# Performance work log

Hardware: AMD Instinct MI355X
Metric: run time of the kernel (lower is better)

## Reference

```python
import jax, jax.numpy as jnp
import numpy as np

DIM = 32
B, H, W = 4, 256, 256


def conv1x1(x, w, b):
    # x: [B,C,H,W], w: [O,C], b: [O]
    return jnp.einsum('bchw,oc->bohw', x, w) + b[None, :, None, None]


def conv3x3(x, w, b):
    # x: [B,C,H,W], w: [O,C,3,3]
    out = jax.lax.conv_general_dilated(
        x, w, window_strides=(1, 1), padding='SAME',
        dimension_numbers=('NCHW', 'OIHW', 'NCHW'))
    return out + b[None, :, None, None]


def fft2d(x):
    # fft2 over last two dims, then fftshift over ALL dims (torch default)
    f = jnp.fft.fftshift(jnp.fft.fft2(x, norm='ortho'))
    return jnp.concatenate([f.real, f.imag], axis=1)  # [B,2C,H,W]


def ifft2d(x):
    f = jnp.fft.ifftshift(x)  # over ALL dims (torch default)
    re, im = jnp.split(f, 2, axis=1)
    c = jax.lax.complex(re, im)
    return jnp.abs(jnp.fft.ifft2(c, norm='ortho'))  # [B,C,H,W]


def setup_inputs() -> dict:
    key = jax.random.key(0)
    ks = jax.random.split(key, 16)
    C = DIM
    s = 0.02  # small init keeps the global-HW dot products in a sane softmax range
    inp = {
        'x': jax.random.normal(ks[0], (B, C, H, W), jnp.float32),
        'y': jax.random.normal(ks[1], (B, C, H, W), jnp.float32),
        'wq': jax.random.normal(ks[2], (C, C), jnp.float32) * s,
        'bq': jnp.zeros((C,), jnp.float32),
        'wk': jax.random.normal(ks[3], (C, C), jnp.float32) * s,
        'bk': jnp.zeros((C,), jnp.float32),
        'wv': jax.random.normal(ks[4], (C, C), jnp.float32) * s,
        'bv': jnp.zeros((C,), jnp.float32),
        'wd': jax.random.normal(ks[5], (C, C), jnp.float32) * s,
        'bd': jnp.zeros((C,), jnp.float32),
        'wc': jax.random.normal(ks[6], (2 * C, 2 * C, 3, 3), jnp.float32) * s,
        'bc': jnp.zeros((2 * C,), jnp.float32),
        'wi': jax.random.normal(ks[7], (2 * C, 2 * C, 3, 3), jnp.float32) * s,
        'bi': jnp.zeros((2 * C,), jnp.float32),
    }
    return inp


def reference(x, y, wq, bq, wk, bk, wv, bv, wd, bd, wc, bc, wi, bi):
    b, c, h, w = x.shape
    xq = conv1x1(x, wq, bq).reshape(b, c, h * w)            # [B,C,HW]
    dft = conv3x3(fft2d(conv1x1(y, wd, bd)), wc, bc)        # [B,2C,H,W]
    yk, yv = jnp.split(dft, 2, axis=1)
    yk = conv1x1(yk, wk, bk).reshape(b, c, h * w)
    yv = conv1x1(yv, wv, bv).reshape(b, c, h * w)
    att = jnp.einsum('bcn,bdn->bcd', xq, yk)                # [B,C,C]
    att = jax.nn.softmax(att, axis=1)                       # softmax over dim=1 (as in torch)
    out = jnp.einsum('bcd,bdn->bcn', att, yv).reshape(b, c, h, w)
    out = out + ifft2d(conv3x3(jax.nn.relu(dft), wi, bi))
    return out
```

## Files before the change

kernel.cpp:

```cpp
#include <hip/hip_runtime.h>
#include <math.h>

#define HW_ (256*256)
#define CH 32
#define CH2 64
#define BATCH 4

typedef short bf16x8 __attribute__((ext_vector_type(8)));
typedef float f32x4 __attribute__((ext_vector_type(4)));

__device__ __forceinline__ unsigned short f2bf(float f) {
    union { float f; unsigned u; } v; v.f = f;
    unsigned r = v.u + 0x7fffu + ((v.u >> 16) & 1u);
    return (unsigned short)(r >> 16);
}
__device__ __forceinline__ float bf2f(unsigned h) {
    union { unsigned u; float f; } v; v.u = h << 16;
    return v.f;
}

__device__ __forceinline__ int ctof_slot(int s) {
    return s < 16 ? s + 16 : s < 32 ? s + 32 : s < 48 ? s - 32 : s - 16;
}

__device__ __forceinline__ void build_tw4(float2* tw, float sign) {
    int tid = threadIdx.x;
    float ang = sign * 6.2831853071795864769f * (float)tid / 256.0f;
    float s, c; sincosf(ang, &s, &c);
    tw[tid] = make_float2(c, s);
}

__device__ __forceinline__ int rev4_8(int i) {
    return ((i & 3) << 6) | ((i & 12) << 2) | ((i & 48) >> 2) | (i >> 6);
}

__device__ __forceinline__ float2 cmul(float2 a, float2 b) {
    return make_float2(a.x*b.x - a.y*b.y, a.x*b.y + a.y*b.x);
}

template<int SGN>
__device__ __forceinline__ void fft_core4(float2* A, const float2* tw) {
    const int tid = threadIdx.x;
    for (int idx = tid; idx < 16*256; idx += 256) {
        int l = idx & 15, i = idx >> 4;
        int j = rev4_8(i);
        if (i < j) {
            int base = l*257;
            float2 t = A[base+i]; A[base+i] = A[base+j]; A[base+j] = t;
        }
    }
    __syncthreads();
    #pragma unroll
    for (int st = 0; st < 4; ++st) {
        const int lq2 = 2*st;
        const int q = 1 << lq2;
        const int estep = 64 >> lq2;
        for (int idx = tid; idx < 16*64; idx += 256) {
            int l = idx & 15, bf = idx >> 4;
            int j = bf & (q-1);
            int g = bf >> lq2;
            int base = l*257 + (g << (lq2+2)) + j;
            float2 x0 = A[base];
            float2 x1 = A[base + q];
            float2 x2 = A[base + 2*q];
            float2 x3 = A[base + 3*q];
            if (st > 0) {
                int e = j * estep;
                x1 = cmul(x1, tw[e]);
                x2 = cmul(x2, tw[2*e]);
                x3 = cmul(x3, tw[3*e]);
            }
            float2 t0 = make_float2(x0.x + x2.x, x0.y + x2.y);
            float2 t1 = make_float2(x0.x - x2.x, x0.y - x2.y);
            float2 t2 = make_float2(x1.x + x3.x, x1.y + x3.y);
            float2 t3 = make_float2(x1.x - x3.x, x1.y - x3.y);
            float2 r  = make_float2(-SGN * t3.y, SGN * t3.x);
            A[base]       = make_float2(t0.x + t2.x, t0.y + t2.y);
            A[base + q]   = make_float2(t1.x + r.x, t1.y + r.y);
            A[base + 2*q] = make_float2(t0.x - t2.x, t0.y - t2.y);
            A[base + 3*q] = make_float2(t1.x - r.x, t1.y - r.y);
        }
        __syncthreads();
    }
}

__global__ __launch_bounds__(256) void k_fft_fwd1(const unsigned short* __restrict__ yd, ushort2* __restrict__ CAt) {
    __shared__ float2 A[16*257];
    __shared__ float2 tw[256];
    build_tw4(tw, -1.0f);
    int blk = blockIdx.x;
    int bc = blk >> 4, h0 = (blk & 15) << 4;
    const float sc = 1.0f/16.0f;
    const unsigned short* src = yd + (size_t)bc*HW_ + (size_t)h0*256;
    for (int idx = threadIdx.x; idx < 16*256; idx += 256) {
        int l = idx >> 8, w = idx & 255;
        A[l*257 + w] = make_float2(bf2f(src[l*256 + w])*sc, 0.0f);
    }
    __syncthreads();
    fft_core4<-1>(A, tw);
    int t = threadIdx.x;
    ushort2* dst = CAt + (size_t)bc*HW_ + (size_t)t*256 + h0;
    #pragma unroll
    for (int l = 0; l < 16; ++l) {
        float2 v = A[l*257 + t];
        dst[l] = make_ushort2(f2bf(v.x), f2bf(v.y));
    }
}

__global__ __launch_bounds__(256) void k_fft_fwd2(const ushort2* __restrict__ CAt, unsigned short* __restrict__ FSH) {
    __shared__ float2 A[16*257];
    __shared__ float2 tw[256];
    build_tw4(tw, -1.0f);
    int blk = blockIdx.x;
    int b = blk >> 9, chalf = (blk >> 8) & 1, w = blk & 255;
    const float sc = 1.0f/16.0f;
    const ushort2* src = CAt + (((size_t)(b*32 + chalf*16))*256 + w)*256;
    for (int idx = threadIdx.x; idx < 16*256; idx += 256) {
        int l = idx >> 8, h = idx & 255;
        ushort2 v = src[(size_t)l*HW_ + h];
        A[l*257 + h] = make_float2(bf2f(v.x)*sc, bf2f(v.y)*sc);
    }
    __syncthreads();
    fft_core4<-1>(A, tw);
    int t = threadIdx.x;
    int bt = (b + 2) & 3;
    int ht = (t + 128) & 255;
    int wt = (w + 128) & 255;
    unsigned short pk[32];
    #pragma unroll
    for (int l = 0; l < 16; ++l) {
        float2 v = A[l*257 + t];
        pk[l]      = f2bf(v.x);
        pk[16 + l] = f2bf(v.y);
    }
    unsigned short* dst = FSH + ((((size_t)bt*256 + ht)*256 + wt)*64 + chalf*32);
    uint4* d4 = (uint4*)dst;
    const uint4* s4 = (const uint4*)pk;
    d4[0] = s4[0]; d4[1] = s4[1]; d4[2] = s4[2]; d4[3] = s4[3];
}

__global__ __launch_bounds__(256) void k_wpack2(const float* __restrict__ wc, const float* __restrict__ wi,
                                                unsigned short* __restrict__ d1, unsigned short* __restrict__ d2) {
    int i = blockIdx.x*256 + threadIdx.x;
    int half = i >= 36864;
    int j = i - half*36864;
    int tap = j >> 12, rem = j & 4095, oc = rem >> 6, s = rem & 63;
    if (half) {
        d2[j] = f2bf(wi[((size_t)(oc*64 + s))*9 + tap]);
    } else {
        int ic = ctof_slot(s);
        d1[j] = f2bf(wc[((size_t)(oc*64 + ic))*9 + tap]);
    }
}

template<int MODE>
__global__ __launch_bounds__(256) void k_conv3(const unsigned short* __restrict__ in_cl,
                                               const unsigned short* __restrict__ wpk,
                                               const float* __restrict__ bias,
                                               unsigned short* __restrict__ outp) {
    __shared__ __align__(16) char Xs[2112*16];
    __shared__ __align__(16) char Ws[1536*16];
    int tid = threadIdx.x;
    int blk = blockIdx.x;
    int wseg = blk & 3, hg = (blk >> 2) & 63, b = blk >> 8;
    int h0 = hg*4, w0 = wseg*64;

    const uint4* wsrc = (const uint4*)wpk;

    for (int gl = tid; gl < 2112; gl += 256) {
        int slot = gl / 528;
        int rem  = gl - slot*528;
        int col  = rem >> 3, hseg = rem & 7;
        int hh = h0 - 1 + slot;
        int wcol = w0 - 1 + col;
        uint4 v = make_uint4(0,0,0,0);
        if (hh >= 0 && hh < 256 && wcol >= 0 && wcol < 256) {
            v = *(const uint4*)(in_cl + (((size_t)(b*256 + hh)*256 + wcol)*64) + hseg*8);
            if (MODE == 1) {
                unsigned* pv = (unsigned*)&v;
                #pragma unroll
                for (int q = 0; q < 4; ++q) {
                    unsigned a = pv[q];
                    unsigned lo = a & 0xffffu, hi = a >> 16;
                    if (lo & 0x8000u) lo = 0;
                    if (hi & 0x8000u) hi = 0;
                    pv[q] = lo | (hi << 16);
                }
            }
        }
        *(uint4*)(Xs + ((gl << 4) ^ ((col & 7) << 4))) = v;
    }
    for (int gw = tid; gw < 1536; gw += 256) {
        int oc = (gw >> 3) & 63;
        *(uint4*)(Ws + ((gw << 4) ^ ((oc & 7) << 4))) = wsrc[gw];
    }
    __syncthreads();

    int lane = tid & 63;
    int wv = tid >> 6;
    int l16 = lane & 15, lq = lane >> 4;

    f32x4 acc[4][4];
    #pragma unroll
    for (int i = 0; i < 4; ++i)
        #pragma unroll
        for (int j = 0; j < 4; ++j) acc[i][j] = (f32x4)0.0f;

    for (int dy = 0; dy < 3; ++dy) {
        if (dy > 0) {
            __syncthreads();
            int k = dy + 3;
            int slot = k & 3;
            int hh = h0 - 1 + k;
            bool hv = hh < 256;
            for (int gl = tid; gl < 528; gl += 256) {
                int col = gl >> 3, hseg = gl & 7;
                int wcol = w0 - 1 + col;
                uint4 v = make_uint4(0,0,0,0);
                if (hv && wcol >= 0 && wcol < 256) {
                    v = *(const uint4*)(in_cl + (((size_t)(b*256 + hh)*256 + wcol)*64) + hseg*8);
                    if (MODE == 1) {
                        unsigned* pv = (unsigned*)&v;
                        #pragma unroll
                        for (int q = 0; q < 4; ++q) {
                            unsigned a = pv[q];
                            unsigned lo = a & 0xffffu, hi = a >> 16;
                            if (lo & 0x8000u) lo = 0;
                            if (hi & 0x8000u) hi = 0;
                            pv[q] = lo | (hi << 16);
                        }
                    }
                }
                int g = slot*528 + gl;
                *(uint4*)(Xs + ((g << 4) ^ ((col & 7) << 4))) = v;
            }
            for (int gw = tid; gw < 1536; gw += 256) {
                int oc = (gw >> 3) & 63;
                *(uint4*)(Ws + ((gw << 4) ^ ((oc & 7) << 4))) = wsrc[dy*1536 + gw];
            }
            __syncthreads();
        }
        int slot = (wv + dy) & 3;
        #pragma unroll
        for (int dx = 0; dx < 3; ++dx) {
            #pragma unroll
            for (int kk = 0; kk < 2; ++kk) {
                int hseg = kk*4 + lq;
                bf16x8 xf[4], wf[4];
                #pragma unroll
                for (int j = 0; j < 4; ++j) {
                    int col = j*16 + l16 + dx;
                    int g = slot*528 + col*8 + hseg;
                    xf[j] = *(const bf16x8*)(Xs + ((g << 4) ^ ((col & 7) << 4)));
                }
                #pragma unroll
                for (int i = 0; i < 4; ++i) {
                    int oc = i*16 + l16;
                    int lw = dx*512 + oc*8 + hseg;
                    wf[i] = *(const bf16x8*)(Ws + ((lw << 4) ^ ((oc & 7) << 4)));
                    #pragma unroll
                    for (int j = 0; j < 4; ++j) {
                        if (MODE == 0)
                            acc[i][j] = __builtin_amdgcn_mfma_f32_16x16x32_bf16(wf[i], xf[j], acc[i][j], 0, 0, 0);
                        else
                            acc[i][j] = __builtin_amdgcn_mfma_f32_16x16x32_bf16(xf[j], wf[i], acc[i][j], 0, 0, 0);
                    }
                }
            }
        }
    }

    int h = h0 + wv;
    if (MODE == 0) {
        #pragma unroll
        for (int j = 0; j < 4; ++j) {
            int px = w0 + j*16 + l16;
            unsigned short* orow = outp + (((size_t)b*256 + h)*256 + px)*64;
            #pragma unroll
            for (int i = 0; i < 4; ++i) {
                int oc0 = i*16 + lq*4;
                float4 bv = *(const float4*)(bias + oc0);
                unsigned short c0 = f2bf(acc[i][j][0] + bv.x);
                unsigned short c1 = f2bf(acc[i][j][1] + bv.y);
                unsigned short c2 = f2bf(acc[i][j][2] + bv.z);
                unsigned short c3 = f2bf(acc[i][j][3] + bv.w);
                uint2 u;
                u.x = (unsigned)c0 | ((unsigned)c1 << 16);
                u.y = (unsigned)c2 | ((unsigned)c3 << 16);
                *(uint2*)(orow + oc0) = u;
            }
        }
    } else {
        #pragma unroll
        for (int i = 0; i < 4; ++i) {
            int oc = i*16 + l16;
            float bv = bias[oc];
            unsigned short* oplane = outp + ((size_t)b*64 + oc)*HW_ + (size_t)h*256;
            #pragma unroll
            for (int j = 0; j < 4; ++j) {
                int px0 = w0 + j*16 + lq*4;
                unsigned short c0 = f2bf(acc[i][j][0] + bv);
                unsigned short c1 = f2bf(acc[i][j][1] + bv);
                unsigned short c2 = f2bf(acc[i][j][2] + bv);
                unsigned short c3 = f2bf(acc[i][j][3] + bv);
                uint2 u;
                u.x = (unsigned)c0 | ((unsigned)c1 << 16);
                u.y = (unsigned)c2 | ((unsigned)c3 << 16);
                *(uint2*)(oplane + px0) = u;
            }
        }
    }
}

__global__ __launch_bounds__(256) void k_conv1x1(const float* __restrict__ in, const float* __restrict__ w,
                                                 const float* __restrict__ bias, unsigned short* __restrict__ out) {
    __shared__ float ts[32*257];
    int blk = blockIdx.x; int b = blk >> 8, h = blk & 255;
    int tid = threadIdx.x;
    const float* src = in + (size_t)b*CH*HW_ + (size_t)h*256;
    for (int idx = tid; idx < 32*256; idx += 256) {
        int c = idx >> 8, ww = idx & 255;
        ts[c*257 + ww] = src[(size_t)c*HW_ + ww];
    }
    __syncthreads();
    float acc[32];
    #pragma unroll
    for (int o = 0; o < 32; ++o) acc[o] = bias[o];
    for (int c = 0; c < 32; ++c) {
        float v = ts[c*257 + tid];
        #pragma unroll
        for (int o = 0; o < 32; ++o) acc[o] += w[o*32 + c] * v;
    }
    unsigned short* dst = out + (size_t)b*CH*HW_ + (size_t)h*256 + tid;
    #pragma unroll
    for (int o = 0; o < 32; ++o) dst[(size_t)o*HW_] = f2bf(acc[o]);
}

__global__ __launch_bounds__(256) void k_gram(const float* __restrict__ x, const unsigned short* __restrict__ dcl,
                                              float* __restrict__ Mpart, float* __restrict__ Sxp, float* __restrict__ Sdp) {
    __shared__ float mred[1024];
    __shared__ float sxred[32];
    __shared__ float sdred[32];
    int blk = blockIdx.x;
    int b = blk >> 7, chunk = blk & 127;
    int tid = threadIdx.x, lane = tid & 63, wv = tid >> 6;
    int l16 = lane & 15, lq = lane >> 4;
    for (int idx = tid; idx < 1024; idx += 256) mred[idx] = 0.0f;
    if (tid < 32) { sxred[tid] = 0.0f; sdred[tid] = 0.0f; }
    __syncthreads();

    const float* xb0 = x + (size_t)b*CH*HW_ + (size_t)l16*HW_;
    const float* xb1 = xb0 + (size_t)16*HW_;
    const unsigned short* db = dcl + (size_t)b*HW_*64;

    f32x4 acc[2][2];
    #pragma unroll
    for (int i = 0; i < 2; ++i)
        #pragma unroll
        for (int j = 0; j < 2; ++j) acc[i][j] = (f32x4)0.0f;
    float sx0 = 0, sx1 = 0, sd0 = 0, sd1 = 0;

    int pxw = chunk*512 + wv*128;
    #pragma unroll
    for (int ks = 0; ks < 4; ++ks) {
        int px = pxw + ks*32 + lq*8;
        float4 xa = *(const float4*)(xb0 + px);
        float4 xc = *(const float4*)(xb0 + px + 4);
        float4 ya = *(const float4*)(xb1 + px);
        float4 yc = *(const float4*)(xb1 + px + 4);
        bf16x8 a0, a1, b0, b1;
        const float* pxa = (const float*)&xa;
        const float* pxc = (const float*)&xc;
        const float* pya = (const float*)&ya;
        const float* pyc = (const float*)&yc;
        #pragma unroll
        for (int j = 0; j < 4; ++j) {
            a0[j]   = (short)f2bf(pxa[j]);  sx0 += pxa[j];
            a0[4+j] = (short)f2bf(pxc[j]);  sx0 += pxc[j];
            a1[j]   = (short)f2bf(pya[j]);  sx1 += pya[j];
            a1[4+j] = (short)f2bf(pyc[j]);  sx1 += pyc[j];
        }
        const unsigned short* dbp = db + (size_t)px*64 + l16;
        #pragma unroll
        for (int j = 0; j < 8; ++j) {
            unsigned short v0 = dbp[j*64];
            unsigned short v1 = dbp[j*64 + 16];
            b0[j] = (short)v0;  sd0 += bf2f(v0);
            b1[j] = (short)v1;  sd1 += bf2f(v1);
        }
        acc[0][0] = __builtin_amdgcn_mfma_f32_16x16x32_bf16(a0, b0, acc[0][0], 0, 0, 0);
        acc[0][1] = __builtin_amdgcn_mfma_f32_16x16x32_bf16(a0, b1, acc[0][1], 0, 0, 0);
        acc[1][0] = __builtin_amdgcn_mfma_f32_16x16x32_bf16(a1, b0, acc[1][0], 0, 0, 0);
        acc[1][1] = __builtin_amdgcn_mfma_f32_16x16x32_bf16(a1, b1, acc[1][1], 0, 0, 0);
    }

    #pragma unroll
    for (int fi = 0; fi < 2; ++fi)
        #pragma unroll
        for (int fj = 0; fj < 2; ++fj)
            #pragma unroll
            for (int r = 0; r < 4; ++r)
                atomicAdd(&mred[(fi*16 + lq*4 + r)*32 + fj*16 + l16], acc[fi][fj][r]);

    sx0 += __shfl_xor(sx0, 16); sx0 += __shfl_xor(sx0, 32);
    sx1 += __shfl_xor(sx1, 16); sx1 += __shfl_xor(sx1, 32);
    sd0 += __shfl_xor(sd0, 16); sd0 += __shfl_xor(sd0, 32);
    sd1 += __shfl_xor(sd1, 16); sd1 += __shfl_xor(sd1, 32);
    if (lane < 16) {
        atomicAdd(&sxred[l16], sx0);
        atomicAdd(&sxred[l16 + 16], sx1);
        atomicAdd(&sdred[l16], sd0);
        atomicAdd(&sdred[l16 + 16], sd1);
    }
    __syncthreads();

    float* mp = Mpart + ((size_t)(b*128 + chunk))*1024;
    for (int idx = tid; idx < 1024; idx += 256) mp[idx] = mred[idx];
    if (tid < 32) {
        Sxp[(b*128 + chunk)*32 + tid] = sxred[tid];
        Sdp[(b*128 + chunk)*32 + tid] = sdred[tid];
    }
}

__global__ __launch_bounds__(256) void k_reduce(const float* __restrict__ Mpart, const float* __restrict__ Sxp,
                                                const float* __restrict__ Sdp,
                                                float* __restrict__ M, float* __restrict__ Sx, float* __restrict__ Sdk) {
    int b = blockIdx.x >> 2, seg = blockIdx.x & 3;
    int o = seg*256 + threadIdx.x;
    float s = 0;
    for (int c = 0; c < 128; ++c) s += Mpart[((size_t)(b*128 + c))*1024 + o];
    M[b*1024 + o] = s;
    if (seg == 0) {
        if (threadIdx.x < 32) {
            float t = 0;
            for (int c = 0; c < 128; ++c) t += Sxp[(b*128 + c)*32 + threadIdx.x];
            Sx[b*32 + threadIdx.x] = t;
        } else if (threadIdx.x < 64) {
            int e = threadIdx.x - 32;
            float t = 0;
            for (int c = 0; c < 128; ++c) t += Sdp[(b*128 + c)*32 + e];
            Sdk[b*32 + e] = t;
        }
    }
}

__global__ __launch_bounds__(256) void k_att(const float* __restrict__ M, const float* __restrict__ Sx,
                                              const float* __restrict__ Sdk,
                                              const float* __restrict__ wq, const float* __restrict__ bq,
                                              const float* __restrict__ wk, const float* __restrict__ bk,
                                              const float* __restrict__ wv, const float* __restrict__ bv,
                                              float* __restrict__ att2, float* __restrict__ sout) {
    __shared__ float Mls[1024], T1[1024], attls[32*33];
    __shared__ float wqs[1024], wks[1024], wvs[1024];
    __shared__ float q1[32], k1[32];
    int tid = threadIdx.x;
    int b = blockIdx.x;
    for (int idx = tid; idx < 1024; idx += 256) {
        wqs[idx] = wq[idx]; wks[idx] = wk[idx]; wvs[idx] = wv[idx];
        Mls[idx] = M[b*1024 + idx];
    }
    __syncthreads();
    if (tid < 32) { float s=0; for (int a=0;a<32;++a) s += wqs[tid*32+a]*Sx[b*32+a]; q1[tid]=s; }
    else if (tid < 64) { int d=tid-32; float s=0; for (int e=0;e<32;++e) s += wks[d*32+e]*Sdk[b*32+e]; k1[d]=s; }
    for (int idx = tid; idx < 1024; idx += 256) {
        int c = idx >> 5, e = idx & 31;
        float s = 0;
        for (int a=0;a<32;++a) s += wqs[c*32+a]*Mls[a*32+e];
        T1[idx] = s;
    }
    __syncthreads();
    for (int idx = tid; idx < 1024; idx += 256) {
        int c = idx >> 5, d = idx & 31;
        float s = 0;
        for (int e=0;e<32;++e) s += T1[c*32+e]*wks[d*32+e];
        s += bq[c]*k1[d] + bk[d]*q1[c] + 65536.0f*bq[c]*bk[d];
        attls[c*33+d] = s;
    }
    __syncthreads();
    if (tid < 32) {
        int d = tid;
        float mx = -1e30f;
        for (int c=0;c<32;++c) mx = fmaxf(mx, attls[c*33+d]);
        float sum = 0;
        for (int c=0;c<32;++c) { float e_ = expf(attls[c*33+d]-mx); attls[c*33+d]=e_; sum+=e_; }
        float inv = 1.0f/sum;
        for (int c=0;c<32;++c) attls[c*33+d] *= inv;
    }
    __syncthreads();
    for (int idx = tid; idx < 1024; idx += 256) {
        int c = idx >> 5, e = idx & 31;
        float s = 0;
        for (int d=0; d<32; ++d) s += attls[c*33+d]*wvs[d*32+e];
        att2[b*1024 + idx] = s;
    }
    if (tid < 32) {
        float s=0; for (int d=0;d<32;++d) s += attls[tid*33+d]*bv[d];
        sout[b*32+tid] = s;
    }
}

__global__ __launch_bounds__(256) void k_fft_inv1(const unsigned short* __restrict__ G, ushort2* __restrict__ Z1T) {
    __shared__ float2 A[16*257];
    __shared__ float2 tw[256];
    build_tw4(tw, 1.0f);
    int blk = blockIdx.x;
    int bc = blk >> 4, w0 = (blk & 15) << 4;
    int b = bc >> 5, c = bc & 31;
    int bs = (b + 2) & 3;
    const float sc = 1.0f/16.0f;
    const unsigned short* gre = G + ((size_t)(bs*CH2 + c + 32))*HW_;
    const unsigned short* gim = G + ((size_t)(bs*CH2 + c))*HW_;
    for (int idx = threadIdx.x; idx < 16*256; idx += 256) {
        int h = idx >> 4, l = idx & 15;
        int hs = (h + 128) & 255;
        int ws = (w0 + l + 128) & 255;
        A[l*257 + h] = make_float2(bf2f(gre[(size_t)hs*256 + ws])*sc, bf2f(gim[(size_t)hs*256 + ws])*sc);
    }
    __syncthreads();
    fft_core4<1>(A, tw);
    ushort2* dst = Z1T + (size_t)bc*HW_;
    for (int idx = threadIdx.x; idx < 16*256; idx += 256) {
        int l = idx >> 8, h = idx & 255;
        float2 v = A[l*257 + h];
        dst[(size_t)(w0 + l)*256 + h] = make_ushort2(f2bf(v.x), f2bf(v.y));
    }
}

__global__ __launch_bounds__(256) void k_fft_inv2(const ushort2* __restrict__ Z1T, float* __restrict__ out) {
    __shared__ float2 A[16*257];
    __shared__ float2 tw[256];
    build_tw4(tw, 1.0f);
    int blk = blockIdx.x;
    int bc = blk >> 4, h0 = (blk & 15) << 4;
    const float sc = 1.0f/16.0f;
    const ushort2* src = Z1T + (size_t)bc*HW_ + h0;
    for (int idx = threadIdx.x; idx < 16*256; idx += 256) {
        int w = idx >> 4, l = idx & 15;
        ushort2 v = src[(size_t)w*256 + l];
        A[l*257 + w] = make_float2(bf2f(v.x)*sc, bf2f(v.y)*sc);
    }
    __syncthreads();
    fft_core4<1>(A, tw);
    float* dst = out + (size_t)bc*HW_ + (size_t)h0*256;
    for (int idx = threadIdx.x; idx < 16*256; idx += 256) {
        int l = idx >> 8, w = idx & 255;
        float2 v = A[l*257 + w];
        dst[l*256 + w] = sqrtf(v.x*v.x + v.y*v.y);
    }
}

__global__ __launch_bounds__(256) void k_out(const unsigned short* __restrict__ dcl, const float* __restrict__ att2,
                                             const float* __restrict__ sv, float* __restrict__ out) {
    __shared__ __align__(16) float A2ls[1024];
    __shared__ float svls[32];
    int blk = blockIdx.x; int b = blk >> 8, h = blk & 255;
    int tid = threadIdx.x;
    for (int idx = tid; idx < 1024; idx += 256) A2ls[idx] = att2[b*1024 + idx];
    if (tid < 32) svls[tid] = sv[b*32 + tid];
    __syncthreads();
    int px = tid;
    const uint4* dvp = (const uint4*)(dcl + ((((size_t)b*256 + h)*256 + px)*64 + 32));
    uint4 d0 = dvp[0], d1 = dvp[1];
    unsigned u[8] = {d0.x, d0.y, d0.z, d0.w, d1.x, d1.y, d1.z, d1.w};
    float dv[32];
    #pragma unroll
    for (int i = 0; i < 8; ++i) {
        dv[2*i]   = bf2f(u[i] & 0xffffu);
        dv[2*i+1] = bf2f(u[i] >> 16);
    }
    float accv[32];
    #pragma unroll
    for (int c = 0; c < 32; ++c) accv[c] = svls[c];
    #pragma unroll
    for (int q = 0; q < 8; ++q) {
        #pragma unroll
        for (int c = 0; c < 32; ++c) {
            float4 a4 = *(const float4*)&A2ls[c*32 + q*4];
            accv[c] += a4.x*dv[q*4] + a4.y*dv[q*4+1] + a4.z*dv[q*4+2] + a4.w*dv[q*4+3];
        }
    }
    float* ob = out + (size_t)b*CH*HW_ + (size_t)h*256 + px;
    #pragma unroll
    for (int c = 0; c < 32; ++c) ob[(size_t)c*HW_] += accv[c];
}

extern "C" void kernel_launch(void* const* d_in, const int* in_sizes, int n_in,
                              void* d_out, int out_size, void* d_ws, size_t ws_size,
                              hipStream_t stream) {
    const float* x  = (const float*)d_in[0];
    const float* y  = (const float*)d_in[1];
    const float* wq = (const float*)d_in[2];
    const float* bq = (const float*)d_in[3];
    const float* wk = (const float*)d_in[4];
    const float* bk = (const float*)d_in[5];
    const float* wv = (const float*)d_in[6];
    const float* bv = (const float*)d_in[7];
    const float* wd = (const float*)d_in[8];
    const float* bd = (const float*)d_in[9];
    const float* wc = (const float*)d_in[10];
    const float* bc = (const float*)d_in[11];
    const float* wi = (const float*)d_in[12];
    const float* bi = (const float*)d_in[13];
    float* out = (float*)d_out;

    char* ws = (char*)d_ws;
    size_t o = 0;
    unsigned short* R1   = (unsigned short*)(ws + o); o += (size_t)BATCH*CH*HW_*2;
    ushort2*        CAt  = (ushort2*)(ws + o);        o += (size_t)BATCH*CH*HW_*4;
    unsigned short* FSHc = (unsigned short*)(ws + o); o += (size_t)BATCH*CH2*HW_*2;
    unsigned short* DFTc = (unsigned short*)(ws + o); o += (size_t)BATCH*CH2*HW_*2;
    unsigned short* Gpl  = (unsigned short*)(ws + o); o += (size_t)BATCH*CH2*HW_*2;
    unsigned short* wpk1 = (unsigned short*)(ws + o); o += 9*64*64*2;
    unsigned short* wpk2 = (unsigned short*)(ws + o); o += 9*64*64*2;
    float*          Mpart= (float*)(ws + o);          o += (size_t)512*1024*4;
    float*          Sxp  = (float*)(ws + o);          o += 512*32*4;
    float*          Sdp  = (float*)(ws + o);          o += 512*32*4;
    float*          Mb   = (float*)(ws + o);          o += 4096*4;
    float*          Sxb  = (float*)(ws + o);          o += 128*4;
    float*          Sdb  = (float*)(ws + o);          o += 128*4;
    float*          A2b  = (float*)(ws + o);          o += 4096*4;
    float*          Svb  = (float*)(ws + o);          o += 128*4;
    if (ws_size < o) return;

    ushort2* Z1T = CAt;

    k_wpack2<<<288, 256, 0, stream>>>(wc, wi, wpk1, wpk2);
    k_conv1x1<<<1024, 256, 0, stream>>>(y, wd, bd, R1);
    k_fft_fwd1<<<2048, 256, 0, stream>>>(R1, CAt);
    k_fft_fwd2<<<2048, 256, 0, stream>>>(CAt, FSHc);
    k_conv3<0><<<1024, 256, 0, stream>>>(FSHc, wpk1, bc, DFTc);
    k_conv3<1><<<1024, 256, 0, stream>>>(DFTc, wpk2, bi, Gpl);
    k_gram<<<512, 256, 0, stream>>>(x, DFTc, Mpart, Sxp, Sdp);
    k_reduce<<<16, 256, 0, stream>>>(Mpart, Sxp, Sdp, Mb, Sxb, Sdb);
    k_att<<<4, 256, 0, stream>>>(Mb, Sxb, Sdb, wq, bq, wk, bk, wv, bv, A2b, Svb);
    k_fft_inv1<<<2048, 256, 0, stream>>>(Gpl, Z1T);
    k_fft_inv2<<<2048, 256, 0, stream>>>(Z1T, out);
    k_out<<<1024, 256, 0, stream>>>(DFTc, A2b, Svb, out);
}
```

Baseline: 284.6 us.

## Register-based 16x16 FFT, direct-weight conv3, fuse reduce into att, bf16 magnitude buffer

Replaces the four-stage shared-memory radix-4 FFT, which had a bit-reversal pass and many barriers, with a two-pass 16x16 decomposition done in registers. Each pass uses one shared-memory transpose with diagonal skew. The 3x3 conv now loads all six input rows into shared memory once and reads weights straight from global memory, dropping the per-dy refill barriers and the weight staging buffer. The k_reduce kernel is folded into k_att. The inverse FFT magnitude is stored as bf16 and added in k_out instead of a read-modify-write of fp32 out. This trades more shared memory and global weight reads, plus extra rounding of the magnitude to bf16, for fewer syncs and fewer launches.

```diff
diff --git a/kernel.cpp b/kernel.cpp
--- a/kernel.cpp
+++ b/kernel.cpp
@@ -21,6 +21,10 @@
 
 __device__ __forceinline__ int ctof_slot(int s) {
     return s < 16 ? s + 16 : s < 32 ? s + 32 : s < 48 ? s - 32 : s - 16;
+}
+
+__device__ __forceinline__ float2 cmul(float2 a, float2 b) {
+    return make_float2(a.x*b.x - a.y*b.y, a.x*b.y + a.y*b.x);
 }
 
 __device__ __forceinline__ void build_tw4(float2* tw, float sign) {
@@ -30,58 +34,63 @@
     tw[tid] = make_float2(c, s);
 }
 
-__device__ __forceinline__ int rev4_8(int i) {
-    return ((i & 3) << 6) | ((i & 12) << 2) | ((i & 48) >> 2) | (i >> 6);
-}
-
-__device__ __forceinline__ float2 cmul(float2 a, float2 b) {
-    return make_float2(a.x*b.x - a.y*b.y, a.x*b.y + a.y*b.x);
-}
-
 template<int SGN>
-__device__ __forceinline__ void fft_core4(float2* A, const float2* tw) {
+__device__ __forceinline__ void fft16_reg(float2* x, const float2* tw) {
+    float2 u[16];
+    #pragma unroll
+    for (int m0 = 0; m0 < 4; ++m0) {
+        float2 x0 = x[m0], x1 = x[m0+4], x2 = x[m0+8], x3 = x[m0+12];
+        float2 t0 = make_float2(x0.x+x2.x, x0.y+x2.y);
+        float2 t1 = make_float2(x0.x-x2.x, x0.y-x2.y);
+        float2 t2 = make_float2(x1.x+x3.x, x1.y+x3.y);
+        float2 t3 = make_float2(x1.x-x3.x, x1.y-x3.y);
+        float2 r  = make_float2(-SGN*t3.y, SGN*t3.x);
+        u[m0*4+0] = make_float2(t0.x+t2.x, t0.y+t2.y);
+        u[m0*4+1] = make_float2(t1.x+r.x,  t1.y+r.y);
+        u[m0*4+2] = make_float2(t0.x-t2.x, t0.y-t2.y);
+        u[m0*4+3] = make_float2(t1.x-r.x,  t1.y-r.y);
+    }
+    #pragma unroll
+    for (int m0 = 1; m0 < 4; ++m0)
+        #pragma unroll
+        for (int a = 1; a < 4; ++a)
+            u[m0*4+a] = cmul(u[m0*4+a], tw[(16*m0*a) & 255]);
+    #pragma unroll
+    for (int a = 0; a < 4; ++a) {
+        float2 x0 = u[a], x1 = u[4+a], x2 = u[8+a], x3 = u[12+a];
+        float2 t0 = make_float2(x0.x+x2.x, x0.y+x2.y);
+        float2 t1 = make_float2(x0.x-x2.x, x0.y-x2.y);
+        float2 t2 = make_float2(x1.x+x3.x, x1.y+x3.y);
+        float2 t3 = make_float2(x1.x-x3.x, x1.y-x3.y);
+        float2 r  = make_float2(-SGN*t3.y, SGN*t3.x);
+        x[a]    = make_float2(t0.x+t2.x, t0.y+t2.y);
+        x[a+4]  = make_float2(t1.x+r.x,  t1.y+r.y);
+        x[a+8]  = make_float2(t0.x-t2.x, t0.y-t2.y);
+        x[a+12] = make_float2(t1.x-r.x,  t1.y-r.y);
+    }
+}
+
+template<int SGN>
+__device__ __forceinline__ void fft_core16(float2* A, const float2* tw) {
     const int tid = threadIdx.x;
-    for (int idx = tid; idx < 16*256; idx += 256) {
-        int l = idx & 15, i = idx >> 4;
-        int j = rev4_8(i);
-        if (i < j) {
-            int base = l*257;
-            float2 t = A[base+i]; A[base+i] = A[base+j]; A[base+j] = t;
-        }
-    }
-    __syncthreads();
-    #pragma unroll
-    for (int st = 0; st < 4; ++st) {
-        const int lq2 = 2*st;
-        const int q = 1 << lq2;
-        const int estep = 64 >> lq2;
-        for (int idx = tid; idx < 16*64; idx += 256) {
-            int l = idx & 15, bf = idx >> 4;
-            int j = bf & (q-1);
-            int g = bf >> lq2;
-            int base = l*257 + (g << (lq2+2)) + j;
-            float2 x0 = A[base];
-            float2 x1 = A[base + q];
-            float2 x2 = A[base + 2*q];
-            float2 x3 = A[base + 3*q];
-            if (st > 0) {
-                int e = j * estep;
-                x1 = cmul(x1, tw[e]);
-                x2 = cmul(x2, tw[2*e]);
-                x3 = cmul(x3, tw[3*e]);
-            }
-            float2 t0 = make_float2(x0.x + x2.x, x0.y + x2.y);
-            float2 t1 = make_float2(x0.x - x2.x, x0.y - x2.y);
-            float2 t2 = make_float2(x1.x + x3.x, x1.y + x3.y);
-            float2 t3 = make_float2(x1.x - x3.x, x1.y - x3.y);
-            float2 r  = make_float2(-SGN * t3.y, SGN * t3.x);
-            A[base]       = make_float2(t0.x + t2.x, t0.y + t2.y);
-            A[base + q]   = make_float2(t1.x + r.x, t1.y + r.y);
-            A[base + 2*q] = make_float2(t0.x - t2.x, t0.y - t2.y);
-            A[base + 3*q] = make_float2(t1.x - r.x, t1.y - r.y);
-        }
-        __syncthreads();
-    }
+    const int l = tid >> 4;
+    const int d = tid & 15;
+    const int base = l*257;
+    float2 x[16];
+    #pragma unroll
+    for (int n1 = 0; n1 < 16; ++n1) x[n1] = A[base + n1*16 + d];
+    fft16_reg<SGN>(x, tw);
+    #pragma unroll
+    for (int k0 = 1; k0 < 16; ++k0) x[k0] = cmul(x[k0], tw[d*k0]);
+    #pragma unroll
+    for (int k0 = 0; k0 < 16; ++k0) A[base + k0*16 + ((d + k0) & 15)] = x[k0];
+    __syncthreads();
+    #pragma unroll
+    for (int n0 = 0; n0 < 16; ++n0) x[n0] = A[base + d*16 + ((n0 + d) & 15)];
+    fft16_reg<SGN>(x, tw);
+    #pragma unroll
+    for (int k1 = 0; k1 < 16; ++k1) A[base + d + k1*16] = x[k1];
+    __syncthreads();
 }
 
 __global__ __launch_bounds__(256) void k_fft_fwd1(const unsigned short* __restrict__ yd, ushort2* __restrict__ CAt) {
@@ -97,7 +106,7 @@
         A[l*257 + w] = make_float2(bf2f(src[l*256 + w])*sc, 0.0f);
     }
     __syncthreads();
-    fft_core4<-1>(A, tw);
+    fft_core16<-1>(A, tw);
     int t = threadIdx.x;
     ushort2* dst = CAt + (size_t)bc*HW_ + (size_t)t*256 + h0;
     #pragma unroll
@@ -121,7 +130,7 @@
         A[l*257 + h] = make_float2(bf2f(v.x)*sc, bf2f(v.y)*sc);
     }
     __syncthreads();
-    fft_core4<-1>(A, tw);
+    fft_core16<-1>(A, tw);
     int t = threadIdx.x;
     int bt = (b + 2) & 3;
     int ht = (t + 128) & 255;
@@ -158,16 +167,13 @@
                                                const unsigned short* __restrict__ wpk,
                                                const float* __restrict__ bias,
                                                unsigned short* __restrict__ outp) {
-    __shared__ __align__(16) char Xs[2112*16];
-    __shared__ __align__(16) char Ws[1536*16];
+    __shared__ __align__(16) char Xs[3168*16];
     int tid = threadIdx.x;
     int blk = blockIdx.x;
     int wseg = blk & 3, hg = (blk >> 2) & 63, b = blk >> 8;
     int h0 = hg*4, w0 = wseg*64;
 
-    const uint4* wsrc = (const uint4*)wpk;
-
-    for (int gl = tid; gl < 2112; gl += 256) {
+    for (int gl = tid; gl < 3168; gl += 256) {
         int slot = gl / 528;
         int rem  = gl - slot*528;
         int col  = rem >> 3, hseg = rem & 7;
@@ -190,10 +196,6 @@
         }
         *(uint4*)(Xs + ((gl << 4) ^ ((col & 7) << 4))) = v;
     }
-    for (int gw = tid; gw < 1536; gw += 256) {
-        int oc = (gw >> 3) & 63;
-        *(uint4*)(Ws + ((gw << 4) ^ ((oc & 7) << 4))) = wsrc[gw];
-    }
     __syncthreads();
 
     int lane = tid & 63;
@@ -206,43 +208,12 @@
         #pragma unroll
         for (int j = 0; j < 4; ++j) acc[i][j] = (f32x4)0.0f;
 
+    #pragma unroll
     for (int dy = 0; dy < 3; ++dy) {
-        if (dy > 0) {
-            __syncthreads();
-            int k = dy + 3;
-            int slot = k & 3;
-            int hh = h0 - 1 + k;
-            bool hv = hh < 256;
-            for (int gl = tid; gl < 528; gl += 256) {
-                int col = gl >> 3, hseg = gl & 7;
-                int wcol = w0 - 1 + col;
-                uint4 v = make_uint4(0,0,0,0);
-                if (hv && wcol >= 0 && wcol < 256) {
-                    v = *(const uint4*)(in_cl + (((size_t)(b*256 + hh)*256 + wcol)*64) + hseg*8);
-                    if (MODE == 1) {
-                        unsigned* pv = (unsigned*)&v;
-                        #pragma unroll
-                        for (int q = 0; q < 4; ++q) {
-                            unsigned a = pv[q];
-                            unsigned lo = a & 0xffffu, hi = a >> 16;
-                            if (lo & 0x8000u) lo = 0;
-                            if (hi & 0x8000u) hi = 0;
-                            pv[q] = lo | (hi << 16);
-                        }
-                    }
-                }
-                int g = slot*528 + gl;
-                *(uint4*)(Xs + ((g << 4) ^ ((col & 7) << 4))) = v;
-            }
-            for (int gw = tid; gw < 1536; gw += 256) {
-                int oc = (gw >> 3) & 63;
-                *(uint4*)(Ws + ((gw << 4) ^ ((oc & 7) << 4))) = wsrc[dy*1536 + gw];
-            }
-            __syncthreads();
-        }
-        int slot = (wv + dy) & 3;
+        int slot = wv + dy;
         #pragma unroll
         for (int dx = 0; dx < 3; ++dx) {
+            int tap = dy*3 + dx;
             #pragma unroll
             for (int kk = 0; kk < 2; ++kk) {
                 int hseg = kk*4 + lq;
@@ -256,8 +227,7 @@
                 #pragma unroll
                 for (int i = 0; i < 4; ++i) {
                     int oc = i*16 + l16;
-                    int lw = dx*512 + oc*8 + hseg;
-                    wf[i] = *(const bf16x8*)(Ws + ((lw << 4) ^ ((oc & 7) << 4)));
+                    wf[i] = *(const bf16x8*)(wpk + (size_t)tap*4096 + oc*64 + hseg*8);
                     #pragma unroll
                     for (int j = 0; j < 4; ++j) {
                         if (MODE == 0)
@@ -422,46 +392,30 @@
     }
 }
 
-__global__ __launch_bounds__(256) void k_reduce(const float* __restrict__ Mpart, const float* __restrict__ Sxp,
-                                                const float* __restrict__ Sdp,
-                                                float* __restrict__ M, float* __restrict__ Sx, float* __restrict__ Sdk) {
-    int b = blockIdx.x >> 2, seg = blockIdx.x & 3;
-    int o = seg*256 + threadIdx.x;
-    float s = 0;
-    for (int c = 0; c < 128; ++c) s += Mpart[((size_t)(b*128 + c))*1024 + o];
-    M[b*1024 + o] = s;
-    if (seg == 0) {
-        if (threadIdx.x < 32) {
-            float t = 0;
-            for (int c = 0; c < 128; ++c) t += Sxp[(b*128 + c)*32 + threadIdx.x];
-            Sx[b*32 + threadIdx.x] = t;
-        } else if (threadIdx.x < 64) {
-            int e = threadIdx.x - 32;
-            float t = 0;
-            for (int c = 0; c < 128; ++c) t += Sdp[(b*128 + c)*32 + e];
-            Sdk[b*32 + e] = t;
-        }
-    }
-}
-
-__global__ __launch_bounds__(256) void k_att(const float* __restrict__ M, const float* __restrict__ Sx,
-                                              const float* __restrict__ Sdk,
+__global__ __launch_bounds__(256) void k_att(const float* __restrict__ Mpart, const float* __restrict__ Sxp,
+                                              const float* __restrict__ Sdp,
                                               const float* __restrict__ wq, const float* __restrict__ bq,
                                               const float* __restrict__ wk, const float* __restrict__ bk,
                                               const float* __restrict__ wv, const float* __restrict__ bv,
                                               float* __restrict__ att2, float* __restrict__ sout) {
     __shared__ float Mls[1024], T1[1024], attls[32*33];
     __shared__ float wqs[1024], wks[1024], wvs[1024];
-    __shared__ float q1[32], k1[32];
+    __shared__ float q1[32], k1[32], sxs[32], sds[32];
     int tid = threadIdx.x;
     int b = blockIdx.x;
-    for (int idx = tid; idx < 1024; idx += 256) {
-        wqs[idx] = wq[idx]; wks[idx] = wk[idx]; wvs[idx] = wv[idx];
-        Mls[idx] = M[b*1024 + idx];
-    }
-    __syncthreads();
-    if (tid < 32) { float s=0; for (int a=0;a<32;++a) s += wqs[tid*32+a]*Sx[b*32+a]; q1[tid]=s; }
-    else if (tid < 64) { int d=tid-32; float s=0; for (int e=0;e<32;++e) s += wks[d*32+e]*Sdk[b*32+e]; k1[d]=s; }
+    for (int idx = tid; idx < 1024; idx += 256) { wqs[idx] = wq[idx]; wks[idx] = wk[idx]; wvs[idx] = wv[idx]; }
+    #pragma unroll
+    for (int q = 0; q < 4; ++q) {
+        int o = tid + q*256;
+        float s = 0;
+        for (int c = 0; c < 128; ++c) s += Mpart[((size_t)(b*128 + c))*1024 + o];
+        Mls[o] = s;
+    }
+    if (tid < 32) { float s = 0; for (int c = 0; c < 128; ++c) s += Sxp[(b*128 + c)*32 + tid]; sxs[tid] = s; }
+    else if (tid < 64) { int e = tid - 32; float s = 0; for (int c = 0; c < 128; ++c) s += Sdp[(b*128 + c)*32 + e]; sds[e] = s; }
+    __syncthreads();
+    if (tid < 32) { float s=0; for (int a=0;a<32;++a) s += wqs[tid*32+a]*sxs[a]; q1[tid]=s; }
+    else if (tid < 64) { int d=tid-32; float s=0; for (int e=0;e<32;++e) s += wks[d*32+e]*sds[e]; k1[d]=s; }
     for (int idx = tid; idx < 1024; idx += 256) {
         int c = idx >> 5, e = idx & 31;
         float s = 0;
@@ -517,7 +471,7 @@
         A[l*257 + h] = make_float2(bf2f(gre[(size_t)hs*256 + ws])*sc, bf2f(gim[(size_t)hs*256 + ws])*sc);
     }
     __syncthreads();
-    fft_core4<1>(A, tw);
+    fft_core16<1>(A, tw);
     ushort2* dst = Z1T + (size_t)bc*HW_;
     for (int idx = threadIdx.x; idx < 16*256; idx += 256) {
         int l = idx >> 8, h = idx & 255;
@@ -526,7 +480,7 @@
     }
 }
 
-__global__ __launch_bounds__(256) void k_fft_inv2(const ushort2* __restrict__ Z1T, float* __restrict__ out) {
+__global__ __launch_bounds__(256) void k_fft_inv2(const ushort2* __restrict__ Z1T, unsigned short* __restrict__ Mag) {
     __shared__ float2 A[16*257];
     __shared__ float2 tw[256];
     build_tw4(tw, 1.0f);
@@ -540,17 +494,18 @@
         A[l*257 + w] = make_float2(bf2f(v.x)*sc, bf2f(v.y)*sc);
     }
     __syncthreads();
-    fft_core4<1>(A, tw);
-    float* dst = out + (size_t)bc*HW_ + (size_t)h0*256;
+    fft_core16<1>(A, tw);
+    unsigned short* dst = Mag + (size_t)bc*HW_ + (size_t)h0*256;
     for (int idx = threadIdx.x; idx < 16*256; idx += 256) {
         int l = idx >> 8, w = idx & 255;
         float2 v = A[l*257 + w];
-        dst[l*256 + w] = sqrtf(v.x*v.x + v.y*v.y);
+        dst[l*256 + w] = f2bf(sqrtf(v.x*v.x + v.y*v.y));
     }
 }
 
 __global__ __launch_bounds__(256) void k_out(const unsigned short* __restrict__ dcl, const float* __restrict__ att2,
-                                             const float* __restrict__ sv, float* __restrict__ out) {
+                                             const float* __restrict__ sv, const unsigned short* __restrict__ Mag,
+                                             float* __restrict__ out) {
     __shared__ __align__(16) float A2ls[1024];
     __shared__ float svls[32];
     int blk = blockIdx.x; int b = blk >> 8, h = blk & 255;
@@ -579,9 +534,10 @@
             accv[c] += a4.x*dv[q*4] + a4.y*dv[q*4+1] + a4.z*dv[q*4+2] + a4.w*dv[q*4+3];
         }
     }
+    const unsigned short* mb = Mag + (size_t)b*CH*HW_ + (size_t)h*256 + px;
     float* ob = out + (size_t)b*CH*HW_ + (size_t)h*256 + px;
     #pragma unroll
-    for (int c = 0; c < 32; ++c) ob[(size_t)c*HW_] += accv[c];
+    for (int c = 0; c < 32; ++c) ob[(size_t)c*HW_] = accv[c] + bf2f(mb[(size_t)c*HW_]);
 }
 
 extern "C" void kernel_launch(void* const* d_in, const int* in_sizes, int n_in,
@@ -615,14 +571,12 @@
     float*          Mpart= (float*)(ws + o);          o += (size_t)512*1024*4;
     float*          Sxp  = (float*)(ws + o);          o += 512*32*4;
     float*          Sdp  = (float*)(ws + o);          o += 512*32*4;
-    float*          Mb   = (float*)(ws + o);          o += 4096*4;
-    float*          Sxb  = (float*)(ws + o);          o += 128*4;
-    float*          Sdb  = (float*)(ws + o);          o += 128*4;
     float*          A2b  = (float*)(ws + o);          o += 4096*4;
     float*          Svb  = (float*)(ws + o);          o += 128*4;
     if (ws_size < o) return;
 
-    ushort2* Z1T = CAt;
+    ushort2*        Z1T = CAt;
+    unsigned short* Mag = R1;
 
     k_wpack2<<<288, 256, 0, stream>>>(wc, wi, wpk1, wpk2);
     k_conv1x1<<<1024, 256, 0, stream>>>(y, wd, bd, R1);
@@ -631,9 +585,8 @@
     k_conv3<0><<<1024, 256, 0, stream>>>(FSHc, wpk1, bc, DFTc);
     k_conv3<1><<<1024, 256, 0, stream>>>(DFTc, wpk2, bi, Gpl);
     k_gram<<<512, 256, 0, stream>>>(x, DFTc, Mpart, Sxp, Sdp);
-    k_reduce<<<16, 256, 0, stream>>>(Mpart, Sxp, Sdp, Mb, Sxb, Sdb);
-    k_att<<<4, 256, 0, stream>>>(Mb, Sxb, Sdb, wq, bq, wk, bk, wv, bv, A2b, Svb);
+    k_att<<<4, 256, 0, stream>>>(Mpart, Sxp, Sdp, wq, bq, wk, bk, wv, bv, A2b, Svb);
     k_fft_inv1<<<2048, 256, 0, stream>>>(Gpl, Z1T);
-    k_fft_inv2<<<2048, 256, 0, stream>>>(Z1T, out);
-    k_out<<<1024, 256, 0, stream>>>(DFTc, A2b, Svb, out);
-}
+    k_fft_inv2<<<2048, 256, 0, stream>>>(Z1T, Mag);
+    k_out<<<1024, 256, 0, stream>>>(DFTc, A2b, Svb, Mag, out);
+}
```

Result: slower. 319.5 us (+12.3%).
